# Performance work log

Measured on AMD Instinct MI355X. Metric: run time of the kernel, lower is better.

The kernel has to match this reference:

```python
import jax, jax.numpy as jnp
import numpy as np

BETA = 0.92
THRESHOLD = 1.0
SLOPE = 25.0  # snntorch surrogate.fast_sigmoid default

T, B, IN_DIM, HID_DIM, OUT_DIM = 1024, 512, 64, 256, 32


@jax.custom_vjp
def spike(mem_shift):
    # heaviside forward, fast-sigmoid surrogate backward
    return (mem_shift > 0).astype(mem_shift.dtype)

def _spike_fwd(mem_shift):
    return spike(mem_shift), mem_shift

def _spike_bwd(mem_shift, g):
    return (g / (SLOPE * jnp.abs(mem_shift) + 1.0) ** 2,)

spike.defvjp(_spike_fwd, _spike_bwd)


def setup_inputs() -> dict:
    key = jax.random.key(0)
    k0, k1, k2, k3, k4 = jax.random.split(key, 5)
    spike_input = jax.random.uniform(k0, (T, B, IN_DIM), dtype=jnp.float32)
    s1 = 1.0 / np.sqrt(IN_DIM)
    s2 = 1.0 / np.sqrt(HID_DIM)
    W1 = jax.random.uniform(k1, (HID_DIM, IN_DIM), jnp.float32, -s1, s1)
    b1 = jax.random.uniform(k2, (HID_DIM,), jnp.float32, -s1, s1)
    W2 = jax.random.uniform(k3, (OUT_DIM, HID_DIM), jnp.float32, -s2, s2)
    b2 = jax.random.uniform(k4, (OUT_DIM,), jnp.float32, -s2, s2)
    return {"spike_input": spike_input, "W1": W1, "b1": b1, "W2": W2, "b2": b2}


def _lif(cur, mem):
    # snntorch Leaky, reset_mechanism='subtract': reset from previous mem, detached
    reset = jax.lax.stop_gradient((mem > THRESHOLD).astype(mem.dtype))
    mem = BETA * mem + cur - reset * THRESHOLD
    spk = spike(mem - THRESHOLD)
    return spk, mem


def reference(spike_input, W1, b1, W2, b2):
    batch = spike_input.shape[1]
    mem1_0 = jnp.zeros((batch, W1.shape[0]), spike_input.dtype)
    mem2_0 = jnp.zeros((batch, W2.shape[0]), spike_input.dtype)

    def step(carry, x_t):
        mem1, mem2 = carry
        cur1 = x_t @ W1.T + b1           # [B, hid]
        spk1, mem1 = _lif(cur1, mem1)
        cur2 = spk1 @ W2.T + b2          # [B, out]
        spk2, mem2 = _lif(cur2, mem2)
        return (mem1, mem2), (spk2, mem2)

    _, (spk2_rec, mem2_rec) = jax.lax.scan(step, (mem1_0, mem2_0), spike_input)
    return spk2_rec, mem2_rec  # each [T, B, out]
```

## Files before the change

### kernel.cpp

```cpp
#include <hip/hip_runtime.h>
#include <stdint.h>

#define T_STEPS 1024
#define BATCH   512
#define IN_DIM  64
#define HID_DIM 256
#define OUT_DIM 32


#define GLOAD_LDS16(GP, LP)                                                \
    __builtin_amdgcn_global_load_lds(                                      \
        (const __attribute__((address_space(1))) void*)(GP),               \
        (__attribute__((address_space(3))) void*)(LP), 16, 0, 0)

#define CHUNK 32

__global__ __launch_bounds__(256, 2) void snn_l1(
    const float* __restrict__ x,
    const float* __restrict__ W1,
    const float* __restrict__ b1,
    unsigned long long* __restrict__ bits)
{
    const int b    = blockIdx.x;
    const int h    = threadIdx.x;
    const int wv   = h >> 6;
    const int lane = h & 63;

    __shared__ __align__(16) float xs[2][CHUNK][IN_DIM];

    float w1r[IN_DIM];
#pragma unroll
    for (int k = 0; k < IN_DIM; ++k) w1r[k] = W1[h * IN_DIM + k];
#pragma unroll
    for (int k = 0; k < IN_DIM; ++k) asm volatile("" : "+v"(w1r[k]));
    const float bias1 = b1[h];

#define STAGE(BUF, CT)                                                     \
    {                                                                      \
        _Pragma("unroll")                                                  \
        for (int r = 0; r < 2; ++r) {                                      \
            const int slot = (r * 4 + wv) * 64 + lane;                     \
            const int step = slot >> 4;                                    \
            const int f4   = slot & 15;                                    \
            const float4* gp = (const float4*)x +                          \
                ((size_t)((CT) * CHUNK + step) * BATCH + b) * 16 + f4;     \
            GLOAD_LDS16(gp, &xs[BUF][0][0] + slot * 4);                    \
        }                                                                  \
    }

    float mem1 = 0.0f;

    STAGE(0, 0)

    for (int c = 0; c < T_STEPS / CHUNK; ++c) {
        const int cb = c & 1;
        __syncthreads();
        if (c + 1 < T_STEPS / CHUNK) STAGE(cb ^ 1, c + 1)

#pragma unroll
        for (int s = 0; s < CHUNK; s += 2) {
            const float4* xp0 = (const float4*)(&xs[cb][s][0]);
            const float4* xp1 = (const float4*)(&xs[cb][s + 1][0]);
            float acc0 = 0.0f, acc1 = 0.0f;
#pragma unroll
            for (int i = 0; i < 16; ++i) {
                const float4 u = xp0[i];
                const float4 v = xp1[i];
                acc0 = fmaf(u.x, w1r[4 * i + 0], acc0);
                acc0 = fmaf(u.y, w1r[4 * i + 1], acc0);
                acc0 = fmaf(u.z, w1r[4 * i + 2], acc0);
                acc0 = fmaf(u.w, w1r[4 * i + 3], acc0);
                acc1 = fmaf(v.x, w1r[4 * i + 0], acc1);
                acc1 = fmaf(v.y, w1r[4 * i + 1], acc1);
                acc1 = fmaf(v.z, w1r[4 * i + 2], acc1);
                acc1 = fmaf(v.w, w1r[4 * i + 3], acc1);
            }
            const int t0 = c * CHUNK + s;
            {
                const float cur1 = __fadd_rn(acc0, bias1);
                const float r1 = (mem1 > 1.0f) ? 1.0f : 0.0f;
                mem1 = __fsub_rn(__fadd_rn(__fmul_rn(0.92f, mem1), cur1), r1);
                const unsigned long long bm = __ballot(mem1 > 1.0f);
                if (lane == 0)
                    bits[((size_t)t0 * BATCH + b) * 4 + wv] = bm;
            }
            {
                const float cur1 = __fadd_rn(acc1, bias1);
                const float r1 = (mem1 > 1.0f) ? 1.0f : 0.0f;
                mem1 = __fsub_rn(__fadd_rn(__fmul_rn(0.92f, mem1), cur1), r1);
                const unsigned long long bm = __ballot(mem1 > 1.0f);
                if (lane == 0)
                    bits[((size_t)(t0 + 1) * BATCH + b) * 4 + wv] = bm;
            }
        }
    }
#undef STAGE
}

__global__ __launch_bounds__(256, 4) void snn_l2gemm(
    const uint32_t* __restrict__ bits,
    const float* __restrict__ W2,
    const float* __restrict__ b2,
    float* __restrict__ cur2)
{
    const int    og = blockIdx.y;
    const size_t tb = (size_t)blockIdx.x * 256 + threadIdx.x;

    const uint4 wA = ((const uint4*)bits)[tb * 2 + 0];
    const uint4 wB = ((const uint4*)bits)[tb * 2 + 1];
    const uint32_t wds[8] = {wA.x, wA.y, wA.z, wA.w, wB.x, wB.y, wB.z, wB.w};

    const float* __restrict__ wr0 = W2 + (og * 4 + 0) * HID_DIM;
    const float* __restrict__ wr1 = W2 + (og * 4 + 1) * HID_DIM;
    const float* __restrict__ wr2 = W2 + (og * 4 + 2) * HID_DIM;
    const float* __restrict__ wr3 = W2 + (og * 4 + 3) * HID_DIM;

    float a0 = 0.0f, a1 = 0.0f, a2 = 0.0f, a3 = 0.0f;

#pragma unroll
    for (int c = 0; c < 16; ++c) {
        float r0[16], r1[16], r2[16], r3[16];
#pragma unroll
        for (int i = 0; i < 16; ++i) {
            const int k = c * 16 + i;
            r0[i] = wr0[k];
            r1[i] = wr1[k];
            r2[i] = wr2[k];
            r3[i] = wr3[k];
        }
        const uint32_t word = wds[c >> 1];
        const int      base = (c & 1) * 16;
#pragma unroll
        for (int i = 0; i < 16; ++i) {
            const float sf = (float)((word >> (base + i)) & 1u);
            a0 = fmaf(sf, r0[i], a0);
            a1 = fmaf(sf, r1[i], a1);
            a2 = fmaf(sf, r2[i], a2);
            a3 = fmaf(sf, r3[i], a3);
        }
    }

    a0 = __fadd_rn(a0, b2[og * 4 + 0]);
    a1 = __fadd_rn(a1, b2[og * 4 + 1]);
    a2 = __fadd_rn(a2, b2[og * 4 + 2]);
    a3 = __fadd_rn(a3, b2[og * 4 + 3]);

    ((float4*)cur2)[tb * (OUT_DIM / 4) + og] = make_float4(a0, a1, a2, a3);
}

__global__ __launch_bounds__(256, 4) void snn_l2scan(
    float* __restrict__ spk_io,
    float* __restrict__ mem_out)
{
    const int tid = threadIdx.x;
    const int o   = tid & (OUT_DIM - 1);
    const int b   = blockIdx.x * 8 + (tid >> 5);

    float* p = spk_io  + (size_t)b * OUT_DIM + o;
    float* m = mem_out + (size_t)b * OUT_DIM + o;
    const size_t step = (size_t)BATCH * OUT_DIM;

    float mem2 = 0.0f;
    for (int t = 0; t < T_STEPS; t += 8) {
        float c[8];
#pragma unroll
        for (int u = 0; u < 8; ++u) c[u] = p[(size_t)(t + u) * step];
#pragma unroll
        for (int u = 0; u < 8; ++u) {
            const float r2 = (mem2 > 1.0f) ? 1.0f : 0.0f;
            mem2 = __fsub_rn(__fadd_rn(__fmul_rn(0.92f, mem2), c[u]), r2);
            p[(size_t)(t + u) * step] = (mem2 > 1.0f) ? 1.0f : 0.0f;
            m[(size_t)(t + u) * step] = mem2;
        }
    }
}

extern "C" void kernel_launch(void* const* d_in, const int* in_sizes, int n_in,
                              void* d_out, int out_size, void* d_ws, size_t ws_size,
                              hipStream_t stream) {
    const float* x  = (const float*)d_in[0];
    const float* W1 = (const float*)d_in[1];
    const float* b1 = (const float*)d_in[2];
    const float* W2 = (const float*)d_in[3];
    const float* b2 = (const float*)d_in[4];

    float* out_spk = (float*)d_out;
    float* out_mem = out_spk + (size_t)T_STEPS * BATCH * OUT_DIM;

    unsigned long long* bits = (unsigned long long*)out_mem;

    snn_l1<<<BATCH, 256, 0, stream>>>(x, W1, b1, bits);

    dim3 g2(T_STEPS * BATCH / 256, 8);
    snn_l2gemm<<<g2, 256, 0, stream>>>((const uint32_t*)bits, W2, b2, out_spk);

    snn_l2scan<<<BATCH / 8, 256, 0, stream>>>(out_spk, out_mem);
}
```

Baseline: 778.9 us.

## Process two batch rows per L1 block with two hidden units per thread

The layer-1 kernel now handles two batch elements per 256-thread block. Each thread holds two hidden-unit weight rows (128 registers) and steps one timestep at a time, so each LDS x read feeds two FMA chains. The grid halves and launch bounds drop to one block per SM. The L2 GEMM now loops over all eight output groups inside one thread, so each thread reads its spike bits once rather than once per grid row. The L2 scan unroll doubles to 16. The risks are fewer resident waves and higher register pressure in L1, and less parallelism in the GEMM.

```diff
diff --git a/kernel.cpp b/kernel.cpp
--- a/kernel.cpp
+++ b/kernel.cpp
@@ -15,40 +15,52 @@
 
 #define CHUNK 32
 
-__global__ __launch_bounds__(256, 2) void snn_l1(
+__global__ __launch_bounds__(256, 1) void snn_l1(
     const float* __restrict__ x,
     const float* __restrict__ W1,
     const float* __restrict__ b1,
     unsigned long long* __restrict__ bits)
 {
-    const int b    = blockIdx.x;
-    const int h    = threadIdx.x;
-    const int wv   = h >> 6;
-    const int lane = h & 63;
-
-    __shared__ __align__(16) float xs[2][CHUNK][IN_DIM];
-
-    float w1r[IN_DIM];
-#pragma unroll
-    for (int k = 0; k < IN_DIM; ++k) w1r[k] = W1[h * IN_DIM + k];
-#pragma unroll
-    for (int k = 0; k < IN_DIM; ++k) asm volatile("" : "+v"(w1r[k]));
-    const float bias1 = b1[h];
+    const int b0   = blockIdx.x * 2;
+    const int tid  = threadIdx.x;
+    const int lane = tid & 63;
+    const int wv   = tid >> 6;
+    const int bl   = tid >> 7;
+    const int hA   = tid & 127;
+    const int hB   = hA + 128;
+    const int b    = b0 + bl;
+
+    __shared__ __align__(16) float xs[2][CHUNK][2][IN_DIM];
+
+    float wA[IN_DIM], wB[IN_DIM];
+#pragma unroll
+    for (int k = 0; k < IN_DIM; ++k) wA[k] = W1[hA * IN_DIM + k];
+#pragma unroll
+    for (int k = 0; k < IN_DIM; ++k) wB[k] = W1[hB * IN_DIM + k];
+#pragma unroll
+    for (int k = 0; k < IN_DIM; ++k) asm volatile("" : "+v"(wA[k]));
+#pragma unroll
+    for (int k = 0; k < IN_DIM; ++k) asm volatile("" : "+v"(wB[k]));
+    const float biasA = b1[hA];
+    const float biasB = b1[hB];
 
 #define STAGE(BUF, CT)                                                     \
     {                                                                      \
         _Pragma("unroll")                                                  \
-        for (int r = 0; r < 2; ++r) {                                      \
-            const int slot = (r * 4 + wv) * 64 + lane;                     \
-            const int step = slot >> 4;                                    \
-            const int f4   = slot & 15;                                    \
+        for (int r = 0; r < 4; ++r) {                                      \
+            const int slot = r * 256 + tid;                                \
+            const int step = slot >> 5;                                    \
+            const int rem  = slot & 31;                                    \
+            const int bb   = rem >> 4;                                     \
+            const int f4   = rem & 15;                                     \
             const float4* gp = (const float4*)x +                          \
-                ((size_t)((CT) * CHUNK + step) * BATCH + b) * 16 + f4;     \
-            GLOAD_LDS16(gp, &xs[BUF][0][0] + slot * 4);                    \
+                ((size_t)((CT) * CHUNK + step) * BATCH + b0 + bb) * 16 + f4; \
+            GLOAD_LDS16(gp, (float*)xs + (size_t)(BUF) * (CHUNK * 2 * IN_DIM) \
+                                + slot * 4);                               \
         }                                                                  \
     }
 
-    float mem1 = 0.0f;
+    float memA = 0.0f, memB = 0.0f;
 
     STAGE(0, 0)
 
@@ -57,40 +69,38 @@
         __syncthreads();
         if (c + 1 < T_STEPS / CHUNK) STAGE(cb ^ 1, c + 1)
 
-#pragma unroll
-        for (int s = 0; s < CHUNK; s += 2) {
-            const float4* xp0 = (const float4*)(&xs[cb][s][0]);
-            const float4* xp1 = (const float4*)(&xs[cb][s + 1][0]);
-            float acc0 = 0.0f, acc1 = 0.0f;
+#pragma unroll 4
+        for (int s = 0; s < CHUNK; ++s) {
+            const float4* xp = (const float4*)(&xs[cb][s][bl][0]);
+            float aA = 0.0f, aB = 0.0f;
 #pragma unroll
             for (int i = 0; i < 16; ++i) {
-                const float4 u = xp0[i];
-                const float4 v = xp1[i];
-                acc0 = fmaf(u.x, w1r[4 * i + 0], acc0);
-                acc0 = fmaf(u.y, w1r[4 * i + 1], acc0);
-                acc0 = fmaf(u.z, w1r[4 * i + 2], acc0);
-                acc0 = fmaf(u.w, w1r[4 * i + 3], acc0);
-                acc1 = fmaf(v.x, w1r[4 * i + 0], acc1);
-                acc1 = fmaf(v.y, w1r[4 * i + 1], acc1);
-                acc1 = fmaf(v.z, w1r[4 * i + 2], acc1);
-                acc1 = fmaf(v.w, w1r[4 * i + 3], acc1);
-            }
-            const int t0 = c * CHUNK + s;
+                const float4 u = xp[i];
+                aA = fmaf(u.x, wA[4 * i + 0], aA);
+                aB = fmaf(u.x, wB[4 * i + 0], aB);
+                aA = fmaf(u.y, wA[4 * i + 1], aA);
+                aB = fmaf(u.y, wB[4 * i + 1], aB);
+                aA = fmaf(u.z, wA[4 * i + 2], aA);
+                aB = fmaf(u.z, wB[4 * i + 2], aB);
+                aA = fmaf(u.w, wA[4 * i + 3], aA);
+                aB = fmaf(u.w, wB[4 * i + 3], aB);
+            }
+            const int t = c * CHUNK + s;
             {
-                const float cur1 = __fadd_rn(acc0, bias1);
-                const float r1 = (mem1 > 1.0f) ? 1.0f : 0.0f;
-                mem1 = __fsub_rn(__fadd_rn(__fmul_rn(0.92f, mem1), cur1), r1);
-                const unsigned long long bm = __ballot(mem1 > 1.0f);
+                const float cur1 = __fadd_rn(aA, biasA);
+                const float r1 = (memA > 1.0f) ? 1.0f : 0.0f;
+                memA = __fsub_rn(__fadd_rn(__fmul_rn(0.92f, memA), cur1), r1);
+                const unsigned long long bm = __ballot(memA > 1.0f);
                 if (lane == 0)
-                    bits[((size_t)t0 * BATCH + b) * 4 + wv] = bm;
+                    bits[((size_t)t * BATCH + b) * 4 + (wv & 1)] = bm;
             }
             {
-                const float cur1 = __fadd_rn(acc1, bias1);
-                const float r1 = (mem1 > 1.0f) ? 1.0f : 0.0f;
-                mem1 = __fsub_rn(__fadd_rn(__fmul_rn(0.92f, mem1), cur1), r1);
-                const unsigned long long bm = __ballot(mem1 > 1.0f);
+                const float cur1 = __fadd_rn(aB, biasB);
+                const float r1 = (memB > 1.0f) ? 1.0f : 0.0f;
+                memB = __fsub_rn(__fadd_rn(__fmul_rn(0.92f, memB), cur1), r1);
+                const unsigned long long bm = __ballot(memB > 1.0f);
                 if (lane == 0)
-                    bits[((size_t)(t0 + 1) * BATCH + b) * 4 + wv] = bm;
+                    bits[((size_t)t * BATCH + b) * 4 + 2 + (wv & 1)] = bm;
             }
         }
     }
@@ -103,49 +113,52 @@
     const float* __restrict__ b2,
     float* __restrict__ cur2)
 {
-    const int    og = blockIdx.y;
     const size_t tb = (size_t)blockIdx.x * 256 + threadIdx.x;
 
-    const uint4 wA = ((const uint4*)bits)[tb * 2 + 0];
-    const uint4 wB = ((const uint4*)bits)[tb * 2 + 1];
-    const uint32_t wds[8] = {wA.x, wA.y, wA.z, wA.w, wB.x, wB.y, wB.z, wB.w};
-
-    const float* __restrict__ wr0 = W2 + (og * 4 + 0) * HID_DIM;
-    const float* __restrict__ wr1 = W2 + (og * 4 + 1) * HID_DIM;
-    const float* __restrict__ wr2 = W2 + (og * 4 + 2) * HID_DIM;
-    const float* __restrict__ wr3 = W2 + (og * 4 + 3) * HID_DIM;
-
-    float a0 = 0.0f, a1 = 0.0f, a2 = 0.0f, a3 = 0.0f;
-
-#pragma unroll
-    for (int c = 0; c < 16; ++c) {
-        float r0[16], r1[16], r2[16], r3[16];
-#pragma unroll
-        for (int i = 0; i < 16; ++i) {
-            const int k = c * 16 + i;
-            r0[i] = wr0[k];
-            r1[i] = wr1[k];
-            r2[i] = wr2[k];
-            r3[i] = wr3[k];
+    const uint4 wAq = ((const uint4*)bits)[tb * 2 + 0];
+    const uint4 wBq = ((const uint4*)bits)[tb * 2 + 1];
+    const uint32_t wds[8] = {wAq.x, wAq.y, wAq.z, wAq.w,
+                             wBq.x, wBq.y, wBq.z, wBq.w};
+
+#pragma unroll 1
+    for (int og = 0; og < 8; ++og) {
+        const float* __restrict__ wr0 = W2 + (og * 4 + 0) * HID_DIM;
+        const float* __restrict__ wr1 = W2 + (og * 4 + 1) * HID_DIM;
+        const float* __restrict__ wr2 = W2 + (og * 4 + 2) * HID_DIM;
+        const float* __restrict__ wr3 = W2 + (og * 4 + 3) * HID_DIM;
+
+        float a0 = 0.0f, a1 = 0.0f, a2 = 0.0f, a3 = 0.0f;
+
+#pragma unroll
+        for (int c = 0; c < 16; ++c) {
+            float r0[16], r1[16], r2[16], r3[16];
+#pragma unroll
+            for (int i = 0; i < 16; ++i) {
+                const int k = c * 16 + i;
+                r0[i] = wr0[k];
+                r1[i] = wr1[k];
+                r2[i] = wr2[k];
+                r3[i] = wr3[k];
+            }
+            const uint32_t word = wds[c >> 1];
+            const int      base = (c & 1) * 16;
+#pragma unroll
+            for (int i = 0; i < 16; ++i) {
+                const float sf = (float)((word >> (base + i)) & 1u);
+                a0 = fmaf(sf, r0[i], a0);
+                a1 = fmaf(sf, r1[i], a1);
+                a2 = fmaf(sf, r2[i], a2);
+                a3 = fmaf(sf, r3[i], a3);
+            }
         }
-        const uint32_t word = wds[c >> 1];
-        const int      base = (c & 1) * 16;
-#pragma unroll
-        for (int i = 0; i < 16; ++i) {
-            const float sf = (float)((word >> (base + i)) & 1u);
-            a0 = fmaf(sf, r0[i], a0);
-            a1 = fmaf(sf, r1[i], a1);
-            a2 = fmaf(sf, r2[i], a2);
-            a3 = fmaf(sf, r3[i], a3);
-        }
-    }
-
-    a0 = __fadd_rn(a0, b2[og * 4 + 0]);
-    a1 = __fadd_rn(a1, b2[og * 4 + 1]);
-    a2 = __fadd_rn(a2, b2[og * 4 + 2]);
-    a3 = __fadd_rn(a3, b2[og * 4 + 3]);
-
-    ((float4*)cur2)[tb * (OUT_DIM / 4) + og] = make_float4(a0, a1, a2, a3);
+
+        a0 = __fadd_rn(a0, b2[og * 4 + 0]);
+        a1 = __fadd_rn(a1, b2[og * 4 + 1]);
+        a2 = __fadd_rn(a2, b2[og * 4 + 2]);
+        a3 = __fadd_rn(a3, b2[og * 4 + 3]);
+
+        ((float4*)cur2)[tb * (OUT_DIM / 4) + og] = make_float4(a0, a1, a2, a3);
+    }
 }
 
 __global__ __launch_bounds__(256, 4) void snn_l2scan(
@@ -161,12 +174,12 @@
     const size_t step = (size_t)BATCH * OUT_DIM;
 
     float mem2 = 0.0f;
-    for (int t = 0; t < T_STEPS; t += 8) {
-        float c[8];
-#pragma unroll
-        for (int u = 0; u < 8; ++u) c[u] = p[(size_t)(t + u) * step];
-#pragma unroll
-        for (int u = 0; u < 8; ++u) {
+    for (int t = 0; t < T_STEPS; t += 16) {
+        float c[16];
+#pragma unroll
+        for (int u = 0; u < 16; ++u) c[u] = p[(size_t)(t + u) * step];
+#pragma unroll
+        for (int u = 0; u < 16; ++u) {
             const float r2 = (mem2 > 1.0f) ? 1.0f : 0.0f;
             mem2 = __fsub_rn(__fadd_rn(__fmul_rn(0.92f, mem2), c[u]), r2);
             p[(size_t)(t + u) * step] = (mem2 > 1.0f) ? 1.0f : 0.0f;
@@ -189,10 +202,10 @@
 
     unsigned long long* bits = (unsigned long long*)out_mem;
 
-    snn_l1<<<BATCH, 256, 0, stream>>>(x, W1, b1, bits);
-
-    dim3 g2(T_STEPS * BATCH / 256, 8);
-    snn_l2gemm<<<g2, 256, 0, stream>>>((const uint32_t*)bits, W2, b2, out_spk);
+    snn_l1<<<BATCH / 2, 256, 0, stream>>>(x, W1, b1, bits);
+
+    snn_l2gemm<<<T_STEPS * BATCH / 256, 256, 0, stream>>>(
+        (const uint32_t*)bits, W2, b2, out_spk);
 
     snn_l2scan<<<BATCH / 8, 256, 0, stream>>>(out_spk, out_mem);
 }
```

New measurement: 2.297 ms. 2.95x slower.
